# Kernel tuning notes

Hardware: AMD Instinct MI355X
Metric: run time of the kernel (lower is better)

Reference implementation:

```python
import jax, jax.numpy as jnp
import numpy as np

GAMMA = 0.99
EPS = 1e-05
K = 8192   # num_embeddings
D = 256    # embed_dim
B, T = 32, 1024

def setup_inputs() -> dict:
    key = jax.random.key(0)
    k1, k2 = jax.random.split(key)
    ze = jax.random.normal(k1, (B, T, D), dtype=jnp.float32)
    embedW = jax.random.normal(k2, (K, D), dtype=jnp.float32)
    mt = jnp.zeros((K, D), dtype=jnp.float32)
    Nt = jnp.zeros((K,), dtype=jnp.float32)
    return {"ze": ze, "embedW": embedW, "mt": mt, "Nt": Nt}

def reference(ze, embedW, mt, Nt):
    b = ze.shape[0]
    ze_flat = ze.reshape(-1, ze.shape[-1])                      # [N, D]
    # squared euclidean distances: ||z||^2 - 2 z W^T + ||w||^2  -> [N, K]
    dist_mat = (jnp.sum(ze_flat * ze_flat, axis=1, keepdims=True)
                - 2.0 * ze_flat @ embedW.T
                + jnp.sum(embedW * embedW, axis=1)[None, :])
    zq_idx = jnp.argmin(dist_mat, axis=-1)                      # [N]
    zq = embedW[zq_idx]                                         # gather [N, D]
    # EMA codebook update (training mode), one-hot scatter expressed as segment sums
    nt = jax.ops.segment_sum(jnp.ones_like(zq_idx, dtype=jnp.float32), zq_idx, num_segments=K)
    Nt_new = GAMMA * Nt + (1.0 - GAMMA) * nt
    st = jax.ops.segment_sum(ze_flat, zq_idx, num_segments=K)   # one_hot.T @ ze
    mt_new = GAMMA * mt + (1.0 - GAMMA) * st
    n = jnp.sum(Nt_new)
    Nn = (Nt_new + EPS) * n / (n + K * EPS)
    embedW_new = mt_new / Nn[:, None]
    zq = zq.reshape(b, -1, zq.shape[-1])                        # [B, T, D]
    zq_idx = zq_idx.reshape(b, -1)                              # [B, T]
    commit = jnp.mean((jax.lax.stop_gradient(zq) - ze) ** 2)
    zq_st = ze + jax.lax.stop_gradient(zq - ze)                 # straight-through
    return (zq_st, commit, zq_idx, embedW_new, mt_new, Nt_new)
```

## Files before the change

### kernel.cpp

```cpp
#include <hip/hip_runtime.h>
#include <cstddef>
#include <cstdint>

#define GAMMA_F 0.99f
#define OMG_F   0.01f
#define EPS_F   1e-5f
#define KN 8192
#define DD 256
#define NN 32768

#define OFF_ZQ     0
#define OFF_COMMIT 8388608
#define OFF_IDX    8388609
#define OFF_EMB    8421377
#define OFF_MT     10518529
#define OFF_NT     12615681

#define C1 16
#define NCH1 (NN / C1)
#define NREC (NCH1 * 2)
#define C2 16
#define NCH2 (NREC / C2)

typedef _Float16 half8 __attribute__((ext_vector_type(8)));
typedef _Float16 half4 __attribute__((ext_vector_type(4)));
typedef float    f32x4 __attribute__((ext_vector_type(4)));
typedef unsigned long long u64;

__device__ __forceinline__ void gload16(const void* g, void* l) {
    __builtin_amdgcn_global_load_lds(
        (const __attribute__((address_space(1))) unsigned int*)g,
        (__attribute__((address_space(3))) unsigned int*)l, 16, 0, 0);
}

__device__ __forceinline__ u64 packdi(float dist, int n) {
    unsigned u = __float_as_uint(dist);
    u ^= (unsigned)((int)u >> 31) | 0x80000000u;
    return ((u64)u << 32) | (unsigned)n;
}

__global__ __launch_bounds__(256) void prep_kernel(
    const float* __restrict__ ze, const float* __restrict__ W,
    _Float16* __restrict__ zh, _Float16* __restrict__ wh,
    float* __restrict__ wsq, unsigned* __restrict__ hist_zero) {
    const int tid = threadIdx.x;
    const size_t gid = (size_t)blockIdx.x * 256 + tid;

    {
        const size_t i0 = gid * 4;
        const float4 v = *(const float4*)(ze + i0);
        half4 h;
        h[0] = (_Float16)v.x; h[1] = (_Float16)v.y;
        h[2] = (_Float16)v.z; h[3] = (_Float16)v.w;
        *(half4*)(zh + i0) = h;
    }
    if (gid < KN) hist_zero[gid] = 0u;

    if (blockIdx.x < KN / 4) {
        const int k = blockIdx.x * 4 + (tid >> 6);
        const int lane = tid & 63;
        const float4 v = *(const float4*)(W + (size_t)k * DD + lane * 4);
        half4 h;
        h[0] = (_Float16)v.x; h[1] = (_Float16)v.y;
        h[2] = (_Float16)v.z; h[3] = (_Float16)v.w;
        *(half4*)(wh + (size_t)k * DD + lane * 4) = h;
        float s = v.x * v.x + v.y * v.y + v.z * v.z + v.w * v.w;
#pragma unroll
        for (int off = 32; off > 0; off >>= 1) s += __shfl_down(s, off, 64);
        if (lane == 0) wsq[k] = s;
    }
}

__global__ __launch_bounds__(256, 4) void screen_kernel(
    const _Float16* __restrict__ zh, const _Float16* __restrict__ wh,
    const float* __restrict__ wsq,
    unsigned* __restrict__ tlo, unsigned* __restrict__ thi) {
    __shared__ __align__(16) _Float16 As[128 * 64];
    __shared__ __align__(16) _Float16 Bs[128 * 64];
    __shared__ __align__(16) u64 top2[128][2];

    const int tid  = threadIdx.x;
    const int wave = tid >> 6;
    const int lane = tid & 63;
    const int quad = lane >> 4;
    const int col  = lane & 15;
    const int ph = wave & 1;
    const int ch = wave >> 1;
    const int pw = ph * 64;
    const int cw = ch * 64;

    const int bm = blockIdx.x >> 6;
    const int bn = blockIdx.x & 63;
    const int m0 = bm * 128;
    const int n0 = bn * 128;

    f32x4 acc[4][4];
#pragma unroll
    for (int i = 0; i < 4; i++)
#pragma unroll
        for (int j = 0; j < 4; j++) acc[i][j] = (f32x4){0.f, 0.f, 0.f, 0.f};

    for (int c = 0; c < 4; ++c) {
        const int d0 = c * 64;
        __syncthreads();
#pragma unroll
        for (int i = 0; i < 4; ++i) {
            const int clin = (wave * 4 + i) * 64 + lane;
            const int mrow = clin >> 3;
            const int p = clin & 7;
            const int q = p ^ (mrow & 7);
            gload16(zh + (size_t)(m0 + mrow) * DD + d0 + q * 8,
                    As + (wave * 4 + i) * 512);
            gload16(wh + (size_t)(n0 + mrow) * DD + d0 + q * 8,
                    Bs + (wave * 4 + i) * 512);
        }
        __syncthreads();

#pragma unroll
        for (int kk = 0; kk < 2; ++kk) {
            half8 a[4], b[4];
#pragma unroll
            for (int t = 0; t < 4; ++t) {
                const int cr = cw + t * 16 + col;
                const int pr = pw + t * 16 + col;
                const int cc = kk * 4 + quad;
                a[t] = *(const half8*)(Bs + cr * 64 + (cc ^ (cr & 7)) * 8);
                b[t] = *(const half8*)(As + pr * 64 + (cc ^ (pr & 7)) * 8);
            }
#pragma unroll
            for (int ci = 0; ci < 4; ++ci)
#pragma unroll
                for (int pj = 0; pj < 4; ++pj)
                    acc[ci][pj] = __builtin_amdgcn_mfma_f32_16x16x32_f16(
                        a[ci], b[pj], acc[ci][pj], 0, 0, 0);
        }
    }

    float wq[4][4];
#pragma unroll
    for (int ci = 0; ci < 4; ++ci) {
        const float4 t = *(const float4*)(wsq + n0 + cw + ci * 16 + quad * 4);
        wq[ci][0] = t.x + 4096.f; wq[ci][1] = t.y + 4096.f;
        wq[ci][2] = t.z + 4096.f; wq[ci][3] = t.w + 4096.f;
    }
    const unsigned base7 = (unsigned)(cw + quad * 4);

#pragma unroll
    for (int pj = 0; pj < 4; ++pj) {
        unsigned t0 = 0xFFFFFFFFu, t1 = 0xFFFFFFFFu;
#pragma unroll
        for (int ci = 0; ci < 4; ++ci)
#pragma unroll
            for (int v = 0; v < 4; ++v) {
                const float dist = fmaf(-2.0f, acc[ci][pj][v], wq[ci][v]);
                const unsigned x = (__float_as_uint(dist) & ~127u) |
                                   (base7 + ci * 16 + v);
                const unsigned mx = t0 > x ? t0 : x;
                t0 = t0 < x ? t0 : x;
                t1 = t1 < mx ? t1 : mx;
            }
#pragma unroll
        for (int mk = 16; mk < 64; mk <<= 1) {
            const unsigned o0 = __shfl_xor(t0, mk, 64);
            const unsigned o1 = __shfl_xor(t1, mk, 64);
            const unsigned lo = t0 < o0 ? t0 : o0;
            const unsigned hi = t0 < o0 ? o0 : t0;
            const unsigned mn = t1 < o1 ? t1 : o1;
            t0 = lo;
            t1 = hi < mn ? hi : mn;
        }
        if (quad == 0)
            top2[pw + pj * 16 + col][ch] = ((u64)t1 << 32) | t0;
    }
    __syncthreads();
    if (tid < 128) {
        const u64 e0 = top2[tid][0], e1 = top2[tid][1];
        const unsigned a0 = (unsigned)e0, a1 = (unsigned)(e0 >> 32);
        const unsigned b0 = (unsigned)e1, b1 = (unsigned)(e1 >> 32);
        const unsigned t0 = a0 < b0 ? a0 : b0;
        const unsigned hi = a0 < b0 ? b0 : a0;
        const unsigned mn = a1 < b1 ? a1 : b1;
        const unsigned t1 = hi < mn ? hi : mn;
        const unsigned c1 = n0 + (t0 & 127u);
        const unsigned c2 = n0 + (t1 & 127u);
        const u64 ent = (u64)(t0 & ~127u) | ((u64)c1 << 32) | ((u64)c2 << 48);
        tlo[(size_t)bn * NN + m0 + tid] = (unsigned)ent;
        thi[(size_t)bn * NN + m0 + tid] = (unsigned)(ent >> 32);
    }
}

__global__ __launch_bounds__(256) void select_kernel(
    const unsigned* __restrict__ tlo, const unsigned* __restrict__ thi,
    const float* __restrict__ ze, const float* __restrict__ W,
    float* __restrict__ idxf, float* __restrict__ zq_out,
    unsigned* __restrict__ hist, float* __restrict__ partials) {
    __shared__ unsigned sl[4][32];
    __shared__ float wsum[4];
    const int tid = threadIdx.x;
    const int lane = tid & 63;
    const int w = tid >> 6;

    const int b = blockIdx.x;
    const int vb = (b & 7) * 1024 + (b >> 3);
    const int n = vb * 4 + w;
    const unsigned elo = tlo[(size_t)lane * NN + n];
    const unsigned ehi = thi[(size_t)lane * NN + n];
    const float d1 = __uint_as_float(elo);
    float mn = d1;
#pragma unroll
    for (int off = 32; off > 0; off >>= 1)
        mn = fminf(mn, __shfl_xor(mn, off, 64));
    const bool q = d1 <= mn + 1.0f;
    const u64 bal = __ballot(q);
    if (q) {
        const int rank = __popcll(bal & ((1ull << lane) - 1ull));
        if (rank < 16) {
            sl[w][2 * rank + 0] = ehi & 0xffffu;
            sl[w][2 * rank + 1] = ehi >> 16;
        }
    }
    unsigned m = 2u * (unsigned)__popcll(bal);
    m = m < 32u ? m : 32u;
    __syncthreads();

    const float4 z = *(const float4*)(ze + (size_t)n * DD + lane * 4);
    u64 best = ~0ull;
    unsigned j = 0;
    for (; j + 2 <= m; j += 2) {
        const unsigned c0 = sl[w][j];
        const unsigned c1 = sl[w][j + 1];
        const float4 w0 = *(const float4*)(W + (size_t)c0 * DD + lane * 4);
        const float4 w1 = *(const float4*)(W + (size_t)c1 * DD + lane * 4);
        float d0 = z.x * w0.x + z.y * w0.y + z.z * w0.z + z.w * w0.w;
        float q0 = w0.x * w0.x + w0.y * w0.y + w0.z * w0.z + w0.w * w0.w;
        float d1c = z.x * w1.x + z.y * w1.y + z.z * w1.z + z.w * w1.w;
        float q1 = w1.x * w1.x + w1.y * w1.y + w1.z * w1.z + w1.w * w1.w;
#pragma unroll
        for (int off = 32; off > 0; off >>= 1) {
            d0  += __shfl_xor(d0, off, 64);
            q0  += __shfl_xor(q0, off, 64);
            d1c += __shfl_xor(d1c, off, 64);
            q1  += __shfl_xor(q1, off, 64);
        }
        const u64 p0 = packdi(fmaf(-2.0f, d0, q0), (int)c0);
        const u64 p1 = packdi(fmaf(-2.0f, d1c, q1), (int)c1);
        const u64 pm = p0 < p1 ? p0 : p1;
        best = best < pm ? best : pm;
    }
    if (j < m) {
        const unsigned c0 = sl[w][j];
        const float4 w0 = *(const float4*)(W + (size_t)c0 * DD + lane * 4);
        float d0 = z.x * w0.x + z.y * w0.y + z.z * w0.z + z.w * w0.w;
        float q0 = w0.x * w0.x + w0.y * w0.y + w0.z * w0.z + w0.w * w0.w;
#pragma unroll
        for (int off = 32; off > 0; off >>= 1) {
            d0 += __shfl_xor(d0, off, 64);
            q0 += __shfl_xor(q0, off, 64);
        }
        const u64 p0 = packdi(fmaf(-2.0f, d0, q0), (int)c0);
        best = best < p0 ? best : p0;
    }
    const int idx = (int)(unsigned)(best & 0xFFFFFFFFull);
    if (lane == 0) {
        idxf[n] = (float)idx;
        atomicAdd(hist + idx, 1u);
    }

    const float4 ww = *(const float4*)(W + (size_t)idx * DD + lane * 4);
    float4 d, o;
    d.x = ww.x - z.x; d.y = ww.y - z.y; d.z = ww.z - z.z; d.w = ww.w - z.w;
    o.x = z.x + d.x; o.y = z.y + d.y; o.z = z.z + d.z; o.w = z.w + d.w;
    *(float4*)(zq_out + (size_t)n * DD + lane * 4) = o;

    float c = d.x * d.x + d.y * d.y + d.z * d.z + d.w * d.w;
#pragma unroll
    for (int off = 32; off > 0; off >>= 1) c += __shfl_down(c, off, 64);

    if (lane == 0) wsum[w] = c;
    __syncthreads();
    if (tid == 0)
        partials[vb] = wsum[0] + wsum[1] + wsum[2] + wsum[3];
}

__global__ __launch_bounds__(256) void prefix_kernel(
    const float* __restrict__ Nt_in, float* __restrict__ ntn,
    const float* __restrict__ partials, float* __restrict__ commit_out,
    unsigned* __restrict__ offsets, float* __restrict__ nws) {
    const int t = threadIdx.x;
    unsigned* hist = (unsigned*)ntn;
    const int base = t * 32;
    unsigned loc[32];
    unsigned sum = 0;
#pragma unroll
    for (int i = 0; i < 32; ++i) { loc[i] = hist[base + i]; sum += loc[i]; }

    __shared__ unsigned ssum[256];
    __shared__ float cred[256];
    __shared__ float fred[256];
    ssum[t] = sum;
    float cp = 0.f;
    for (int i = t; i < NN / 4; i += 256) cp += partials[i];
    cred[t] = cp;
    __syncthreads();

    for (int off = 1; off < 256; off <<= 1) {
        const unsigned v = (t >= off) ? ssum[t - off] : 0u;
        __syncthreads();
        ssum[t] += v;
        __syncthreads();
    }
    unsigned run = (t > 0) ? ssum[t - 1] : 0u;

    for (int off = 128; off > 0; off >>= 1) {
        if (t < off) cred[t] += cred[t + off];
        __syncthreads();
    }
    if (t == 0) *commit_out = cred[0] * (1.0f / 8388608.0f);

#pragma unroll
    for (int i = 0; i < 32; ++i) {
        offsets[base + i] = run;
        run += loc[i];
    }
    float fs = 0.f;
#pragma unroll
    for (int i = 0; i < 32; ++i) {
        const float v = GAMMA_F * Nt_in[base + i] + OMG_F * (float)loc[i];
        ntn[base + i] = v;
        fs += v;
    }
    fred[t] = fs;
    __syncthreads();
    for (int off = 128; off > 0; off >>= 1) {
        if (t < off) fred[t] += fred[t + off];
        __syncthreads();
    }
    if (t == 0) nws[0] = fred[0];
}

__global__ __launch_bounds__(256) void scatter_kernel(
    const float* __restrict__ idxf, unsigned* __restrict__ offsets,
    unsigned* __restrict__ perm, unsigned* __restrict__ codes,
    float* __restrict__ s_zero) {
    const size_t gid = (size_t)blockIdx.x * 256 + threadIdx.x;
    *(float4*)(s_zero + gid * 4) = (float4){0.f, 0.f, 0.f, 0.f};
    if (gid < NN) {
        const int idx = (int)idxf[gid];
        const unsigned pos = atomicAdd(offsets + idx, 1u);
        perm[pos] = (unsigned)gid;
        codes[pos] = (unsigned)idx;
    }
}

__global__ __launch_bounds__(256) void mt1_kernel(
    const float* __restrict__ ze,
    const unsigned* __restrict__ perm, const unsigned* __restrict__ codes,
    float* __restrict__ s_out, unsigned* __restrict__ prec,
    float* __restrict__ pdata) {
    const int tid = threadIdx.x;
    const int lane = tid & 63;
    const int w = blockIdx.x * 4 + (tid >> 6);
    const int j0 = w * C1;

    unsigned ccur = codes[j0];
    bool first = true;
    float4 acc = {0.f, 0.f, 0.f, 0.f};

    for (int j = j0; j < j0 + C1; ++j) {
        const unsigned c = codes[j];
        if (c != ccur) {
            if (first) {
                *(float4*)(pdata + (size_t)(2 * w) * DD + lane * 4) = acc;
                if (lane == 0) prec[2 * w] = ccur;
                first = false;
            } else {
                float4 r;
                r.x = OMG_F * acc.x; r.y = OMG_F * acc.y;
                r.z = OMG_F * acc.z; r.w = OMG_F * acc.w;
                *(float4*)(s_out + (size_t)ccur * DD + lane * 4) = r;
            }
            acc = (float4){0.f, 0.f, 0.f, 0.f};
            ccur = c;
        }
        const unsigned p = perm[j];
        const float4 z = *(const float4*)(ze + (size_t)p * DD + lane * 4);
        acc.x += z.x; acc.y += z.y; acc.z += z.z; acc.w += z.w;
    }
    if (first) {
        *(float4*)(pdata + (size_t)(2 * w) * DD + lane * 4) = acc;
        *(float4*)(pdata + (size_t)(2 * w + 1) * DD + lane * 4) =
            (float4){0.f, 0.f, 0.f, 0.f};
        if (lane == 0) { prec[2 * w] = ccur; prec[2 * w + 1] = ccur; }
    } else {
        *(float4*)(pdata + (size_t)(2 * w + 1) * DD + lane * 4) = acc;
        if (lane == 0) prec[2 * w + 1] = ccur;
    }
}

__global__ __launch_bounds__(256) void mt2_kernel(
    const unsigned* __restrict__ prec,
    const float* __restrict__ pdata, float* __restrict__ s_out) {
    const int tid = threadIdx.x;
    const int lane = tid & 63;
    const int w = blockIdx.x * 4 + (tid >> 6);
    const int r0 = w * C2;

    unsigned ccur = prec[r0];
    bool first = true;
    float4 acc = {0.f, 0.f, 0.f, 0.f};

    for (int r = r0; r < r0 + C2; ++r) {
        const unsigned c = prec[r];
        if (c != ccur) {
            if (first) {
                float* mp = s_out + (size_t)ccur * DD + lane * 4;
                atomicAdd(mp + 0, OMG_F * acc.x);
                atomicAdd(mp + 1, OMG_F * acc.y);
                atomicAdd(mp + 2, OMG_F * acc.z);
                atomicAdd(mp + 3, OMG_F * acc.w);
                first = false;
            } else {
                float4 rr;
                rr.x = OMG_F * acc.x; rr.y = OMG_F * acc.y;
                rr.z = OMG_F * acc.z; rr.w = OMG_F * acc.w;
                *(float4*)(s_out + (size_t)ccur * DD + lane * 4) = rr;
            }
            acc = (float4){0.f, 0.f, 0.f, 0.f};
            ccur = c;
        }
        const float4 v = *(const float4*)(pdata + (size_t)r * DD + lane * 4);
        acc.x += v.x; acc.y += v.y; acc.z += v.z; acc.w += v.w;
    }
    float* mp = s_out + (size_t)ccur * DD + lane * 4;
    atomicAdd(mp + 0, OMG_F * acc.x);
    atomicAdd(mp + 1, OMG_F * acc.y);
    atomicAdd(mp + 2, OMG_F * acc.z);
    atomicAdd(mp + 3, OMG_F * acc.w);
}

__global__ __launch_bounds__(256) void final_kernel(
    const float* __restrict__ nt_new, const float* __restrict__ mt_in,
    float* __restrict__ mt_new, const float* __restrict__ nws,
    float* __restrict__ emb_out) {
    const float n = nws[0];
    const size_t i0 = ((size_t)blockIdx.x * 256 + threadIdx.x) * 4;
    const int k = (int)(i0 >> 8);

    const float4 s = *(const float4*)(mt_new + i0);
    const float4 m = *(const float4*)(mt_in + i0);
    float4 r;
    r.x = GAMMA_F * m.x + s.x;
    r.y = GAMMA_F * m.y + s.y;
    r.z = GAMMA_F * m.z + s.z;
    r.w = GAMMA_F * m.w + s.w;
    *(float4*)(mt_new + i0) = r;

    const float Nn = (nt_new[k] + EPS_F) * n / (n + (float)KN * EPS_F);
    float4 e;
    e.x = r.x / Nn;
    e.y = r.y / Nn;
    e.z = r.z / Nn;
    e.w = r.w / Nn;
    *(float4*)(emb_out + i0) = e;
}

extern "C" void kernel_launch(void* const* d_in, const int* in_sizes, int n_in,
                              void* d_out, int out_size, void* d_ws, size_t ws_size,
                              hipStream_t stream) {
    const float* ze = (const float*)d_in[0];
    const float* W  = (const float*)d_in[1];
    const float* mt = (const float*)d_in[2];
    const float* Nt = (const float*)d_in[3];

    float* out    = (float*)d_out;
    float* zq_out = out + OFF_ZQ;
    float* commit = out + OFF_COMMIT;
    float* idxf   = out + OFF_IDX;
    float* emb    = out + OFF_EMB;
    float* mtn    = out + OFF_MT;
    float* ntn    = out + OFF_NT;

    _Float16* zh = (_Float16*)zq_out;
    _Float16* wh = (_Float16*)(zq_out + (size_t)NN * DD / 2);
    float* wsqbuf = zq_out + (size_t)NN * DD / 2 + (size_t)KN * DD / 2;
    unsigned* tlo = (unsigned*)emb;
    unsigned* thi = tlo + (size_t)64 * NN;
    unsigned* offsets = tlo;
    unsigned* perm    = tlo + 8192;
    unsigned* codes   = tlo + 40960;
    unsigned* prec    = tlo + 73728;
    float*    pdata   = (float*)tlo + 77827;
    unsigned* hist    = (unsigned*)ntn;
    float*    nws      = (float*)d_ws;
    float*    partials = (float*)d_ws + 4;

    prep_kernel<<<(NN * DD / 4) / 256, 256, 0, stream>>>(
        ze, W, zh, wh, wsqbuf, hist);

    screen_kernel<<<(NN / 128) * (KN / 128), 256, 0, stream>>>(
        zh, wh, wsqbuf, tlo, thi);

    select_kernel<<<NN / 4, 256, 0, stream>>>(
        tlo, thi, ze, W, idxf, zq_out, hist, partials);

    prefix_kernel<<<1, 256, 0, stream>>>(Nt, ntn, partials, commit,
                                         offsets, nws);

    scatter_kernel<<<(KN * DD / 4) / 256, 256, 0, stream>>>(
        idxf, offsets, perm, codes, mtn);

    mt1_kernel<<<NCH1 / 4, 256, 0, stream>>>(ze, perm, codes, mtn,
                                             prec, pdata);

    mt2_kernel<<<NCH2 / 4, 256, 0, stream>>>(prec, pdata, mtn);

    final_kernel<<<(KN * DD / 4) / 256, 256, 0, stream>>>(ntn, mt, mtn,
                                                          nws, emb);
}
```

Baseline: 337.9 us.

## Fuse tail kernels into one cooperative kernel with grid syncs

Replaces the five tail launches (prefix, scatter, mt1, mt2, final) with a single cooperative kernel of 1024 blocks that uses grid.sync between phases. It also zeroes the mt buffer at kernel start and runs the prefix on block 0. The goal is to remove launch overhead and inter-kernel gaps. The cost is grid-wide barriers, a serial single-block prefix while the other blocks wait, and lower parallelism in some phases.

```diff
diff --git a/kernel.cpp b/kernel.cpp
--- a/kernel.cpp
+++ b/kernel.cpp
@@ -1,6 +1,9 @@
 #include <hip/hip_runtime.h>
+#include <hip/hip_cooperative_groups.h>
 #include <cstddef>
 #include <cstdint>
+
+namespace cg = cooperative_groups;
 
 #define GAMMA_F 0.99f
 #define OMG_F   0.01f
@@ -282,186 +285,178 @@
         partials[vb] = wsum[0] + wsum[1] + wsum[2] + wsum[3];
 }
 
-__global__ __launch_bounds__(256) void prefix_kernel(
-    const float* __restrict__ Nt_in, float* __restrict__ ntn,
-    const float* __restrict__ partials, float* __restrict__ commit_out,
-    unsigned* __restrict__ offsets, float* __restrict__ nws) {
+__global__ __launch_bounds__(256, 4) void tail_kernel(
+    const float* Nt_in, float* ntn, const float* partials,
+    float* commit_out, unsigned* offsets, float* nws,
+    const float* idxf, unsigned* perm, unsigned* codes,
+    float* s_out , const float* ze, const float* mt_in,
+    float* emb_out, unsigned* prec, float* pdata) {
+    cg::grid_group grid = cg::this_grid();
     const int t = threadIdx.x;
-    unsigned* hist = (unsigned*)ntn;
-    const int base = t * 32;
-    unsigned loc[32];
-    unsigned sum = 0;
-#pragma unroll
-    for (int i = 0; i < 32; ++i) { loc[i] = hist[base + i]; sum += loc[i]; }
+    const int gtid = blockIdx.x * 256 + t;
+    const int lane = t & 63;
+    const int wv = gtid >> 6;
 
     __shared__ unsigned ssum[256];
     __shared__ float cred[256];
     __shared__ float fred[256];
-    ssum[t] = sum;
-    float cp = 0.f;
-    for (int i = t; i < NN / 4; i += 256) cp += partials[i];
-    cred[t] = cp;
-    __syncthreads();
-
-    for (int off = 1; off < 256; off <<= 1) {
-        const unsigned v = (t >= off) ? ssum[t - off] : 0u;
+
+    {
+        *(float4*)(s_out + (size_t)gtid * 4) = (float4){0.f, 0.f, 0.f, 0.f};
+        *(float4*)(s_out + (size_t)(gtid + 262144) * 4) =
+            (float4){0.f, 0.f, 0.f, 0.f};
+    }
+    if (blockIdx.x == 0) {
+        unsigned* hist = (unsigned*)ntn;
+        const int base = t * 32;
+        unsigned loc[32];
+        unsigned sum = 0;
+#pragma unroll
+        for (int i = 0; i < 32; ++i) { loc[i] = hist[base + i]; sum += loc[i]; }
+        ssum[t] = sum;
+        float cp = 0.f;
+        for (int i = t; i < NN / 4; i += 256) cp += partials[i];
+        cred[t] = cp;
         __syncthreads();
-        ssum[t] += v;
+        for (int off = 1; off < 256; off <<= 1) {
+            const unsigned v = (t >= off) ? ssum[t - off] : 0u;
+            __syncthreads();
+            ssum[t] += v;
+            __syncthreads();
+        }
+        unsigned run = (t > 0) ? ssum[t - 1] : 0u;
+        for (int off = 128; off > 0; off >>= 1) {
+            if (t < off) cred[t] += cred[t + off];
+            __syncthreads();
+        }
+        if (t == 0) *commit_out = cred[0] * (1.0f / 8388608.0f);
+#pragma unroll
+        for (int i = 0; i < 32; ++i) {
+            offsets[base + i] = run;
+            run += loc[i];
+        }
+        float fs = 0.f;
+#pragma unroll
+        for (int i = 0; i < 32; ++i) {
+            const float v = GAMMA_F * Nt_in[base + i] + OMG_F * (float)loc[i];
+            ntn[base + i] = v;
+            fs += v;
+        }
+        fred[t] = fs;
         __syncthreads();
-    }
-    unsigned run = (t > 0) ? ssum[t - 1] : 0u;
-
-    for (int off = 128; off > 0; off >>= 1) {
-        if (t < off) cred[t] += cred[t + off];
-        __syncthreads();
-    }
-    if (t == 0) *commit_out = cred[0] * (1.0f / 8388608.0f);
-
-#pragma unroll
-    for (int i = 0; i < 32; ++i) {
-        offsets[base + i] = run;
-        run += loc[i];
-    }
-    float fs = 0.f;
-#pragma unroll
-    for (int i = 0; i < 32; ++i) {
-        const float v = GAMMA_F * Nt_in[base + i] + OMG_F * (float)loc[i];
-        ntn[base + i] = v;
-        fs += v;
-    }
-    fred[t] = fs;
-    __syncthreads();
-    for (int off = 128; off > 0; off >>= 1) {
-        if (t < off) fred[t] += fred[t + off];
-        __syncthreads();
-    }
-    if (t == 0) nws[0] = fred[0];
-}
-
-__global__ __launch_bounds__(256) void scatter_kernel(
-    const float* __restrict__ idxf, unsigned* __restrict__ offsets,
-    unsigned* __restrict__ perm, unsigned* __restrict__ codes,
-    float* __restrict__ s_zero) {
-    const size_t gid = (size_t)blockIdx.x * 256 + threadIdx.x;
-    *(float4*)(s_zero + gid * 4) = (float4){0.f, 0.f, 0.f, 0.f};
-    if (gid < NN) {
-        const int idx = (int)idxf[gid];
+        for (int off = 128; off > 0; off >>= 1) {
+            if (t < off) fred[t] += fred[t + off];
+            __syncthreads();
+        }
+        if (t == 0) nws[0] = fred[0];
+    }
+    grid.sync();
+
+    if (gtid < NN) {
+        const int idx = (int)idxf[gtid];
         const unsigned pos = atomicAdd(offsets + idx, 1u);
-        perm[pos] = (unsigned)gid;
+        perm[pos] = (unsigned)gtid;
         codes[pos] = (unsigned)idx;
     }
-}
-
-__global__ __launch_bounds__(256) void mt1_kernel(
-    const float* __restrict__ ze,
-    const unsigned* __restrict__ perm, const unsigned* __restrict__ codes,
-    float* __restrict__ s_out, unsigned* __restrict__ prec,
-    float* __restrict__ pdata) {
-    const int tid = threadIdx.x;
-    const int lane = tid & 63;
-    const int w = blockIdx.x * 4 + (tid >> 6);
-    const int j0 = w * C1;
-
-    unsigned ccur = codes[j0];
-    bool first = true;
-    float4 acc = {0.f, 0.f, 0.f, 0.f};
-
-    for (int j = j0; j < j0 + C1; ++j) {
-        const unsigned c = codes[j];
-        if (c != ccur) {
-            if (first) {
-                *(float4*)(pdata + (size_t)(2 * w) * DD + lane * 4) = acc;
-                if (lane == 0) prec[2 * w] = ccur;
-                first = false;
-            } else {
-                float4 r;
-                r.x = OMG_F * acc.x; r.y = OMG_F * acc.y;
-                r.z = OMG_F * acc.z; r.w = OMG_F * acc.w;
-                *(float4*)(s_out + (size_t)ccur * DD + lane * 4) = r;
+    grid.sync();
+
+    if (wv < NCH1) {
+        const int w = wv;
+        const int j0 = w * C1;
+        unsigned ccur = codes[j0];
+        bool first = true;
+        float4 acc = {0.f, 0.f, 0.f, 0.f};
+        for (int j = j0; j < j0 + C1; ++j) {
+            const unsigned c = codes[j];
+            if (c != ccur) {
+                if (first) {
+                    *(float4*)(pdata + (size_t)(2 * w) * DD + lane * 4) = acc;
+                    if (lane == 0) prec[2 * w] = ccur;
+                    first = false;
+                } else {
+                    float4 r;
+                    r.x = OMG_F * acc.x; r.y = OMG_F * acc.y;
+                    r.z = OMG_F * acc.z; r.w = OMG_F * acc.w;
+                    *(float4*)(s_out + (size_t)ccur * DD + lane * 4) = r;
+                }
+                acc = (float4){0.f, 0.f, 0.f, 0.f};
+                ccur = c;
             }
-            acc = (float4){0.f, 0.f, 0.f, 0.f};
-            ccur = c;
-        }
-        const unsigned p = perm[j];
-        const float4 z = *(const float4*)(ze + (size_t)p * DD + lane * 4);
-        acc.x += z.x; acc.y += z.y; acc.z += z.z; acc.w += z.w;
-    }
-    if (first) {
-        *(float4*)(pdata + (size_t)(2 * w) * DD + lane * 4) = acc;
-        *(float4*)(pdata + (size_t)(2 * w + 1) * DD + lane * 4) =
-            (float4){0.f, 0.f, 0.f, 0.f};
-        if (lane == 0) { prec[2 * w] = ccur; prec[2 * w + 1] = ccur; }
-    } else {
-        *(float4*)(pdata + (size_t)(2 * w + 1) * DD + lane * 4) = acc;
-        if (lane == 0) prec[2 * w + 1] = ccur;
-    }
-}
-
-__global__ __launch_bounds__(256) void mt2_kernel(
-    const unsigned* __restrict__ prec,
-    const float* __restrict__ pdata, float* __restrict__ s_out) {
-    const int tid = threadIdx.x;
-    const int lane = tid & 63;
-    const int w = blockIdx.x * 4 + (tid >> 6);
-    const int r0 = w * C2;
-
-    unsigned ccur = prec[r0];
-    bool first = true;
-    float4 acc = {0.f, 0.f, 0.f, 0.f};
-
-    for (int r = r0; r < r0 + C2; ++r) {
-        const unsigned c = prec[r];
-        if (c != ccur) {
-            if (first) {
-                float* mp = s_out + (size_t)ccur * DD + lane * 4;
-                atomicAdd(mp + 0, OMG_F * acc.x);
-                atomicAdd(mp + 1, OMG_F * acc.y);
-                atomicAdd(mp + 2, OMG_F * acc.z);
-                atomicAdd(mp + 3, OMG_F * acc.w);
-                first = false;
-            } else {
-                float4 rr;
-                rr.x = OMG_F * acc.x; rr.y = OMG_F * acc.y;
-                rr.z = OMG_F * acc.z; rr.w = OMG_F * acc.w;
-                *(float4*)(s_out + (size_t)ccur * DD + lane * 4) = rr;
+            const unsigned p = perm[j];
+            const float4 z = *(const float4*)(ze + (size_t)p * DD + lane * 4);
+            acc.x += z.x; acc.y += z.y; acc.z += z.z; acc.w += z.w;
+        }
+        if (first) {
+            *(float4*)(pdata + (size_t)(2 * w) * DD + lane * 4) = acc;
+            *(float4*)(pdata + (size_t)(2 * w + 1) * DD + lane * 4) =
+                (float4){0.f, 0.f, 0.f, 0.f};
+            if (lane == 0) { prec[2 * w] = ccur; prec[2 * w + 1] = ccur; }
+        } else {
+            *(float4*)(pdata + (size_t)(2 * w + 1) * DD + lane * 4) = acc;
+            if (lane == 0) prec[2 * w + 1] = ccur;
+        }
+    }
+    grid.sync();
+
+    if (wv < NCH2) {
+        const int w = wv;
+        const int r0 = w * C2;
+        unsigned ccur = prec[r0];
+        bool first = true;
+        float4 acc = {0.f, 0.f, 0.f, 0.f};
+        for (int r = r0; r < r0 + C2; ++r) {
+            const unsigned c = prec[r];
+            if (c != ccur) {
+                if (first) {
+                    float* mp = s_out + (size_t)ccur * DD + lane * 4;
+                    atomicAdd(mp + 0, OMG_F * acc.x);
+                    atomicAdd(mp + 1, OMG_F * acc.y);
+                    atomicAdd(mp + 2, OMG_F * acc.z);
+                    atomicAdd(mp + 3, OMG_F * acc.w);
+                    first = false;
+                } else {
+                    float4 rr;
+                    rr.x = OMG_F * acc.x; rr.y = OMG_F * acc.y;
+                    rr.z = OMG_F * acc.z; rr.w = OMG_F * acc.w;
+                    *(float4*)(s_out + (size_t)ccur * DD + lane * 4) = rr;
+                }
+                acc = (float4){0.f, 0.f, 0.f, 0.f};
+                ccur = c;
             }
-            acc = (float4){0.f, 0.f, 0.f, 0.f};
-            ccur = c;
-        }
-        const float4 v = *(const float4*)(pdata + (size_t)r * DD + lane * 4);
-        acc.x += v.x; acc.y += v.y; acc.z += v.z; acc.w += v.w;
-    }
-    float* mp = s_out + (size_t)ccur * DD + lane * 4;
-    atomicAdd(mp + 0, OMG_F * acc.x);
-    atomicAdd(mp + 1, OMG_F * acc.y);
-    atomicAdd(mp + 2, OMG_F * acc.z);
-    atomicAdd(mp + 3, OMG_F * acc.w);
-}
-
-__global__ __launch_bounds__(256) void final_kernel(
-    const float* __restrict__ nt_new, const float* __restrict__ mt_in,
-    float* __restrict__ mt_new, const float* __restrict__ nws,
-    float* __restrict__ emb_out) {
-    const float n = nws[0];
-    const size_t i0 = ((size_t)blockIdx.x * 256 + threadIdx.x) * 4;
-    const int k = (int)(i0 >> 8);
-
-    const float4 s = *(const float4*)(mt_new + i0);
-    const float4 m = *(const float4*)(mt_in + i0);
-    float4 r;
-    r.x = GAMMA_F * m.x + s.x;
-    r.y = GAMMA_F * m.y + s.y;
-    r.z = GAMMA_F * m.z + s.z;
-    r.w = GAMMA_F * m.w + s.w;
-    *(float4*)(mt_new + i0) = r;
-
-    const float Nn = (nt_new[k] + EPS_F) * n / (n + (float)KN * EPS_F);
-    float4 e;
-    e.x = r.x / Nn;
-    e.y = r.y / Nn;
-    e.z = r.z / Nn;
-    e.w = r.w / Nn;
-    *(float4*)(emb_out + i0) = e;
+            const float4 v = *(const float4*)(pdata + (size_t)r * DD + lane * 4);
+            acc.x += v.x; acc.y += v.y; acc.z += v.z; acc.w += v.w;
+        }
+        float* mp = s_out + (size_t)ccur * DD + lane * 4;
+        atomicAdd(mp + 0, OMG_F * acc.x);
+        atomicAdd(mp + 1, OMG_F * acc.y);
+        atomicAdd(mp + 2, OMG_F * acc.z);
+        atomicAdd(mp + 3, OMG_F * acc.w);
+    }
+    grid.sync();
+
+    {
+        const float n = nws[0];
+#pragma unroll
+        for (int it = 0; it < 2; ++it) {
+            const size_t i0 = ((size_t)gtid + (size_t)it * 262144) * 4;
+            const int k = (int)(i0 >> 8);
+            const float4 s = *(const float4*)(s_out + i0);
+            const float4 m = *(const float4*)(mt_in + i0);
+            float4 r;
+            r.x = GAMMA_F * m.x + s.x;
+            r.y = GAMMA_F * m.y + s.y;
+            r.z = GAMMA_F * m.z + s.z;
+            r.w = GAMMA_F * m.w + s.w;
+            *(float4*)(s_out + i0) = r;
+            const float Nn = (ntn[k] + EPS_F) * n / (n + (float)KN * EPS_F);
+            float4 e;
+            e.x = r.x / Nn;
+            e.y = r.y / Nn;
+            e.z = r.z / Nn;
+            e.w = r.w / Nn;
+            *(float4*)(emb_out + i0) = e;
+        }
+    }
 }
 
 extern "C" void kernel_launch(void* const* d_in, const int* in_sizes, int n_in,
@@ -503,17 +498,16 @@
     select_kernel<<<NN / 4, 256, 0, stream>>>(
         tlo, thi, ze, W, idxf, zq_out, hist, partials);
 
-    prefix_kernel<<<1, 256, 0, stream>>>(Nt, ntn, partials, commit,
-                                         offsets, nws);
-
-    scatter_kernel<<<(KN * DD / 4) / 256, 256, 0, stream>>>(
-        idxf, offsets, perm, codes, mtn);
-
-    mt1_kernel<<<NCH1 / 4, 256, 0, stream>>>(ze, perm, codes, mtn,
-                                             prec, pdata);
-
-    mt2_kernel<<<NCH2 / 4, 256, 0, stream>>>(prec, pdata, mtn);
-
-    final_kernel<<<(KN * DD / 4) / 256, 256, 0, stream>>>(ntn, mt, mtn,
-                                                          nws, emb);
-}
+    {
+        const float* Nt_a = Nt;
+        const float* ze_a = ze;
+        const float* mt_a = mt;
+        void* args[] = {
+            (void*)&Nt_a, (void*)&ntn, (void*)&partials, (void*)&commit,
+            (void*)&offsets, (void*)&nws, (void*)&idxf, (void*)&perm,
+            (void*)&codes, (void*)&mtn, (void*)&ze_a, (void*)&mt_a,
+            (void*)&emb, (void*)&prec, (void*)&pdata};
+        hipLaunchCooperativeKernel((void*)tail_kernel, dim3(1024), dim3(256),
+                                   args, 0, stream);
+    }
+}
```

Measured after the change: 775.4 us. +129.5%, slower.
